# Optimization experiments

Hardware: AMD Instinct MI355X
Metric: run time of the kernel (lower is better)

The kernel has to match this reference:

```python
import jax, jax.numpy as jnp
import numpy as np

B, DIN, DOUT, DC, K, DB = 4096, 512, 512, 64, 16, 256
NEG = 0.01
LN_EPS = 1e-5

def _lrelu(v):
    return jnp.where(v >= 0, v, NEG * v)

def setup_inputs() -> dict:
    key = jax.random.key(0)
    ks = jax.random.split(key, 12)
    bound = 1.0 / np.sqrt(DIN)
    def u(k, shape, b):
        return jax.random.uniform(k, shape, jnp.float32, -b, b)
    return {
        "x": jax.random.normal(ks[0], (B, DIN), jnp.float32),
        "c": jax.random.normal(ks[1], (B, DC), jnp.float32),
        "ln_gamma": jnp.ones((DIN,), jnp.float32),
        "ln_beta": jnp.zeros((DIN,), jnp.float32),
        "w1": u(ks[2], (DC, DB), 1.0 / np.sqrt(DC)),
        "b1": u(ks[3], (DB,), 1.0 / np.sqrt(DC)),
        "wr": u(ks[4], (DB, DB), 1.0 / np.sqrt(DB)),
        "br": u(ks[5], (DB,), 1.0 / np.sqrt(DB)),
        "w2": u(ks[6], (DB, K), 1.0 / np.sqrt(DB)),
        "b2": u(ks[7], (K,), 1.0 / np.sqrt(DB)),
        "W": u(ks[8], (K, DIN, DOUT), bound),
        "bvec": u(ks[9], (K, DOUT), bound),
    }

def reference(x, c, ln_gamma, ln_beta, w1, b1, wr, br, w2, b2, W, bvec):
    # DenseActivation: LayerNorm + LeakyReLU (dropout_rate=0)
    mu = jnp.mean(x, axis=-1, keepdims=True)
    var = jnp.mean(jnp.square(x - mu), axis=-1, keepdims=True)
    xn = (x - mu) * jax.lax.rsqrt(var + LN_EPS) * ln_gamma + ln_beta
    a = _lrelu(xn)  # [B, DIN]
    # basis_functions(c): Linear -> 1 preactivation resnet block -> LeakyReLU -> Linear
    h = c @ w1 + b1                      # [B, DB]
    h = h + (_lrelu(h) @ wr + br)        # residual block (preactivation)
    h = _lrelu(h)                        # activate_output
    bf = h @ w2 + b2                     # [B, K]
    # out_b = x_b^T (sum_k bf_bk W_k) + bf_b @ bias ; reordered contraction
    xw = jnp.einsum("bi,kio->bko", a, W)       # [B, K, DOUT]
    out = jnp.einsum("bk,bko->bo", bf, xw)     # [B, DOUT]
    out = out + bf @ bvec
    return out
```

## Files before the change

### kernel.cpp

```cpp
#include <hip/hip_runtime.h>


#define LRELU(v) ((v) >= 0.f ? (v) : 0.01f * (v))

typedef _Float16 f16x8 __attribute__((ext_vector_type(8)));
typedef float f32x4 __attribute__((ext_vector_type(4)));

#define GL16(gp, lp) __builtin_amdgcn_global_load_lds(                      \
    (const __attribute__((address_space(1))) void*)(gp),                    \
    (__attribute__((address_space(3))) void*)(lp), 16, 0, 0)

#define MFMA16(a, b, c) __builtin_amdgcn_mfma_f32_16x16x32_f16((a), (b), (c), 0, 0, 0)

__global__ __launch_bounds__(256) void prep_kernel(
    const float* __restrict__ x, const float* __restrict__ gam,
    const float* __restrict__ bet, _Float16* __restrict__ a,
    const float* __restrict__ c, const float* __restrict__ w1,
    const float* __restrict__ b1, const float* __restrict__ wr,
    const float* __restrict__ br, const float* __restrict__ w2,
    const float* __restrict__ b2, float* __restrict__ bfo,
    const float* __restrict__ W, _Float16* __restrict__ Wt)
{
    __shared__ __align__(16) char smem[18432];
    int tid = threadIdx.x;
    int blk = blockIdx.x;

    if (blk < 512) {
        float* c_l  = (float*)smem;
        float* lr_l = (float*)(smem + 2048);
        float* h_l  = (float*)(smem + 10240);
        int b0 = blk * 8;

        for (int i = tid; i < 8 * 64; i += 256) c_l[i] = c[(size_t)b0 * 64 + i];

        float w1c[64];
#pragma unroll
        for (int u = 0; u < 64; ++u) w1c[u] = w1[u * 256 + tid];
        float b1s = b1[tid];
        __syncthreads();

        float h1[8];
#pragma unroll
        for (int r = 0; r < 8; ++r) h1[r] = b1s;
#pragma unroll
        for (int j4 = 0; j4 < 16; ++j4) {
#pragma unroll
            for (int r = 0; r < 8; ++r) {
                float4 cv = *(const float4*)&c_l[r * 64 + j4 * 4];
                h1[r] += cv.x * w1c[j4 * 4 + 0] + cv.y * w1c[j4 * 4 + 1] +
                         cv.z * w1c[j4 * 4 + 2] + cv.w * w1c[j4 * 4 + 3];
            }
        }
#pragma unroll
        for (int r = 0; r < 8; ++r) lr_l[r * 256 + tid] = LRELU(h1[r]);
        __syncthreads();

        float brv = br[tid];
        float h2[8];
#pragma unroll
        for (int r = 0; r < 8; ++r) h2[r] = h1[r] + brv;

#pragma unroll 1
        for (int jc = 0; jc < 8; ++jc) {
            float w8[32];
#pragma unroll
            for (int u = 0; u < 32; ++u) w8[u] = wr[(jc * 32 + u) * 256 + tid];
#pragma unroll
            for (int j4 = 0; j4 < 8; ++j4) {
#pragma unroll
                for (int r = 0; r < 8; ++r) {
                    float4 lv = *(const float4*)&lr_l[r * 256 + jc * 32 + j4 * 4];
                    h2[r] += lv.x * w8[j4 * 4 + 0] + lv.y * w8[j4 * 4 + 1] +
                             lv.z * w8[j4 * 4 + 2] + lv.w * w8[j4 * 4 + 3];
                }
            }
        }
#pragma unroll
        for (int r = 0; r < 8; ++r) h_l[r * 256 + tid] = LRELU(h2[r]);
        __syncthreads();

        if (tid < 128) {
            int r = tid >> 4, k = tid & 15;
            float s = b2[k];
#pragma unroll 1
            for (int qc = 0; qc < 8; ++qc) {
                float wv[32];
#pragma unroll
                for (int u = 0; u < 32; ++u) wv[u] = w2[(qc * 32 + u) * 16 + k];
#pragma unroll
                for (int q4 = 0; q4 < 8; ++q4) {
                    float4 hv = *(const float4*)&h_l[r * 256 + qc * 32 + q4 * 4];
                    s += hv.x * wv[q4 * 4 + 0] + hv.y * wv[q4 * 4 + 1] +
                         hv.z * wv[q4 * 4 + 2] + hv.w * wv[q4 * 4 + 3];
                }
            }
            bfo[(size_t)(b0 + r) * 16 + k] = s;
        }

    } else if (blk < 1536) {
        float* t = (float*)smem;
        int bid = blk - 512;
        int k  = bid >> 6;
        int it = (bid >> 3) & 7;
        int ot = bid & 7;
        int i0 = it * 64, o0 = ot * 64;

        int rr = tid >> 4, c4 = (tid & 15) * 4;
#pragma unroll
        for (int p = 0; p < 4; ++p) {
            int r = p * 16 + rr;
            float4 v = *(const float4*)&W[((size_t)(k * 512 + i0 + r)) * 512 + o0 + c4];
            t[r * 65 + c4 + 0] = v.x;
            t[r * 65 + c4 + 1] = v.y;
            t[r * 65 + c4 + 2] = v.z;
            t[r * 65 + c4 + 3] = v.w;
        }
        __syncthreads();

        int ol = tid >> 2, c0 = (tid & 3) * 16;
        _Float16 hb[16] __attribute__((aligned(16)));
#pragma unroll
        for (int u = 0; u < 16; ++u) hb[u] = (_Float16)t[(c0 + u) * 65 + ol];
        _Float16* dst = &Wt[(size_t)(o0 + ol) * 8192 + k * 512 + i0 + c0];
        *(float4*)dst       = *(const float4*)&hb[0];
        *(float4*)(dst + 8) = *(const float4*)&hb[8];

    } else {
        int lane = tid & 63;
        int row  = (blk - 1536) * 4 + (tid >> 6);
        const float* xr = x + (size_t)row * 512 + lane * 8;
        float4 v0 = *(const float4*)xr;
        float4 v1 = *(const float4*)(xr + 4);

        float s = v0.x + v0.y + v0.z + v0.w + v1.x + v1.y + v1.z + v1.w;
#pragma unroll
        for (int m = 1; m < 64; m <<= 1) s += __shfl_xor(s, m);
        float mean = s * (1.f / 512.f);

        float d, s2 = 0.f;
        d = v0.x - mean; s2 += d * d;
        d = v0.y - mean; s2 += d * d;
        d = v0.z - mean; s2 += d * d;
        d = v0.w - mean; s2 += d * d;
        d = v1.x - mean; s2 += d * d;
        d = v1.y - mean; s2 += d * d;
        d = v1.z - mean; s2 += d * d;
        d = v1.w - mean; s2 += d * d;
#pragma unroll
        for (int m = 1; m < 64; m <<= 1) s2 += __shfl_xor(s2, m);
        float rstd = rsqrtf(s2 * (1.f / 512.f) + 1e-5f);

        float4 g0 = *(const float4*)&gam[lane * 8];
        float4 g1 = *(const float4*)&gam[lane * 8 + 4];
        float4 b0 = *(const float4*)&bet[lane * 8];
        float4 b1v = *(const float4*)&bet[lane * 8 + 4];

        _Float16 o8[8] __attribute__((aligned(16)));
        float y;
        y = (v0.x - mean) * rstd * g0.x + b0.x;  y = LRELU(y); o8[0] = (_Float16)y;
        y = (v0.y - mean) * rstd * g0.y + b0.y;  y = LRELU(y); o8[1] = (_Float16)y;
        y = (v0.z - mean) * rstd * g0.z + b0.z;  y = LRELU(y); o8[2] = (_Float16)y;
        y = (v0.w - mean) * rstd * g0.w + b0.w;  y = LRELU(y); o8[3] = (_Float16)y;
        y = (v1.x - mean) * rstd * g1.x + b1v.x; y = LRELU(y); o8[4] = (_Float16)y;
        y = (v1.y - mean) * rstd * g1.y + b1v.y; y = LRELU(y); o8[5] = (_Float16)y;
        y = (v1.z - mean) * rstd * g1.z + b1v.z; y = LRELU(y); o8[6] = (_Float16)y;
        y = (v1.w - mean) * rstd * g1.w + b1v.w; y = LRELU(y); o8[7] = (_Float16)y;

        *(float4*)&a[(size_t)row * 512 + lane * 8] = *(const float4*)o8;
    }
}

template <int NSPLIT>
__global__ __launch_bounds__(512, 2) void gemm_kernel(
    const _Float16* __restrict__ A,
    const _Float16* __restrict__ Wt,
    const float* __restrict__ bfg,
    float* __restrict__ pout)
{
    constexpr int KTN = 16 / NSPLIT;
    constexpr int NT  = KTN * 8;

    __shared__ _Float16 As[2][256 * 64];
    __shared__ _Float16 Bs[2][256 * 64];

    const int tid = threadIdx.x;
    const int bid = blockIdx.x;
    const int split = bid % NSPLIT;
    const int mn  = bid / NSPLIT;
    const int n0  = (mn & 1) * 256;
    const int bm0 = (mn >> 1) * 256;
    const int kt0 = split * KTN;

    const int lane = tid & 63, wid = tid >> 6;
    const int wm = wid >> 2, wn = wid & 3;
    const int l16 = lane & 15, lg = lane >> 4;

    _Float16 s16[KTN][8];
#pragma unroll
    for (int kt = 0; kt < KTN; ++kt)
#pragma unroll
        for (int f = 0; f < 8; ++f)
            s16[kt][f] = (_Float16)
                bfg[(size_t)(bm0 + wm * 128 + f * 16 + l16) * 16 + kt0 + kt];

    const int brow = tid >> 3;
    const int bc   = tid & 7;
    const int swc  = bc ^ (brow & 7);
    const _Float16* aAs = A  + (size_t)(bm0 + brow) * 512  + swc * 8;
    const _Float16* aBs = Wt + (size_t)(n0  + brow) * 8192 + swc * 8;

    auto STAGE = [&](int t, int buf) {
        const int ka = (t & 7) * 64;
        const size_t kb = (size_t)(kt0 + (t >> 3)) * 512 + ka;
        char* la = (char*)&As[buf][0] + tid * 16;
        char* lb = (char*)&Bs[buf][0] + tid * 16;
#pragma unroll
        for (int p = 0; p < 4; ++p) {
            GL16(aAs + (size_t)(p * 64) * 512 + ka, la + p * 8192);
            GL16(aBs + (size_t)(p * 64) * 8192 + kb, lb + p * 8192);
        }
    };

    const int swr = l16 & 7;
    const int aRowByte = (wm * 128 + l16) * 128;
    const int bRowByte = (wn * 64 + l16) * 128;
    const int sw0 = ((0 + lg) ^ swr) << 4;
    const int sw1 = ((4 + lg) ^ swr) << 4;

    const f32x4 z4 = {0.f, 0.f, 0.f, 0.f};
    f32x4 acc[8][4];
#pragma unroll
    for (int f = 0; f < 8; ++f)
#pragma unroll
        for (int nf = 0; nf < 4; ++nf) acc[f][nf] = z4;

    STAGE(0, 0);
    STAGE(1, 1);
    asm volatile("s_waitcnt vmcnt(8)" ::: "memory");
    __builtin_amdgcn_s_barrier();
    __builtin_amdgcn_sched_barrier(0);

#pragma unroll
    for (int kt = 0; kt < KTN; ++kt) {
#pragma unroll 1
        for (int t2 = 0; t2 < 8; ++t2) {
            const int t = kt * 8 + t2;
            const int cur = t & 1;
            const char* Ab = (const char*)&As[cur][0];
            const char* Bb = (const char*)&Bs[cur][0];

            f16x8 b8[4][2];
#pragma unroll
            for (int nf = 0; nf < 4; ++nf) {
                b8[nf][0] = *(const f16x8*)(Bb + bRowByte + nf * 2048 + sw0);
                b8[nf][1] = *(const f16x8*)(Bb + bRowByte + nf * 2048 + sw1);
            }

#pragma unroll
            for (int q = 0; q < 4; ++q) {
                f16x8 a0k0 = *(const f16x8*)(Ab + aRowByte + (2 * q + 0) * 2048 + sw0);
                f16x8 a0k1 = *(const f16x8*)(Ab + aRowByte + (2 * q + 0) * 2048 + sw1);
                f16x8 a1k0 = *(const f16x8*)(Ab + aRowByte + (2 * q + 1) * 2048 + sw0);
                f16x8 a1k1 = *(const f16x8*)(Ab + aRowByte + (2 * q + 1) * 2048 + sw1);
                const _Float16 sc0 = s16[kt][2 * q + 0];
                const _Float16 sc1 = s16[kt][2 * q + 1];
                a0k0 *= sc0; a0k1 *= sc0;
                a1k0 *= sc1; a1k1 *= sc1;
                __builtin_amdgcn_s_setprio(1);
#pragma unroll
                for (int nf = 0; nf < 4; ++nf) {
                    acc[2 * q + 0][nf] = MFMA16(a0k0, b8[nf][0], acc[2 * q + 0][nf]);
                    acc[2 * q + 0][nf] = MFMA16(a0k1, b8[nf][1], acc[2 * q + 0][nf]);
                    acc[2 * q + 1][nf] = MFMA16(a1k0, b8[nf][0], acc[2 * q + 1][nf]);
                    acc[2 * q + 1][nf] = MFMA16(a1k1, b8[nf][1], acc[2 * q + 1][nf]);
                }
                __builtin_amdgcn_s_setprio(0);
            }

            __builtin_amdgcn_sched_barrier(0);
            __builtin_amdgcn_s_barrier();
            __builtin_amdgcn_sched_barrier(0);

            if (t + 2 < NT) {
                STAGE(t + 2, cur);
                asm volatile("s_waitcnt vmcnt(8)" ::: "memory");
            } else {
                asm volatile("s_waitcnt vmcnt(0)" ::: "memory");
            }
            __builtin_amdgcn_s_barrier();
            __builtin_amdgcn_sched_barrier(0);
        }
    }

    float* op = pout + (size_t)split * (4096 * 512);
#pragma unroll
    for (int f = 0; f < 8; ++f)
#pragma unroll
        for (int j = 0; j < 4; ++j) {
            const int grow = bm0 + wm * 128 + f * 16 + lg * 4 + j;
            float* orow = op + (size_t)grow * 512 + n0 + wn * 64 + l16;
#pragma unroll
            for (int nf = 0; nf < 4; ++nf)
                orow[nf * 16] = acc[f][nf][j];
        }
}

__global__ __launch_bounds__(256) void reduce_kernel(const float* __restrict__ p,
                                                     const float* __restrict__ bfg,
                                                     const float* __restrict__ bvec,
                                                     float* __restrict__ out,
                                                     int nsplit)
{
    size_t i = (size_t)blockIdx.x * 256 + threadIdx.x;
    const float4* p4 = (const float4*)p;
    float4 s = p4[i];
    for (int sp = 1; sp < nsplit; ++sp) {
        float4 v = p4[i + (size_t)sp * 524288];
        s.x += v.x; s.y += v.y; s.z += v.z; s.w += v.w;
    }
    int b = (int)(i >> 7);
    int c = (int)(i & 127);
    const float* bfr = bfg + (size_t)b * 16;
    const float4* bv4 = (const float4*)bvec;
#pragma unroll
    for (int k = 0; k < 16; ++k) {
        float bk = bfr[k];
        float4 v = bv4[k * 128 + c];
        s.x += bk * v.x; s.y += bk * v.y; s.z += bk * v.z; s.w += bk * v.w;
    }
    ((float4*)out)[i] = s;
}

extern "C" void kernel_launch(void* const* d_in, const int* in_sizes, int n_in,
                              void* d_out, int out_size, void* d_ws, size_t ws_size,
                              hipStream_t stream)
{
    const float* x    = (const float*)d_in[0];
    const float* c    = (const float*)d_in[1];
    const float* gam  = (const float*)d_in[2];
    const float* bet  = (const float*)d_in[3];
    const float* w1   = (const float*)d_in[4];
    const float* b1   = (const float*)d_in[5];
    const float* wr   = (const float*)d_in[6];
    const float* br   = (const float*)d_in[7];
    const float* w2   = (const float*)d_in[8];
    const float* b2   = (const float*)d_in[9];
    const float* W    = (const float*)d_in[10];
    const float* bvec = (const float*)d_in[11];
    float* out = (float*)d_out;

    const size_t outBytes  = (size_t)4096 * 512 * 4;
    const size_t miscBytes = (8u << 20) + (4u << 20) + (256u << 10);

    int nsplit = (ws_size >= 8 * outBytes + miscBytes) ? 8 : 4;

    char* ws = (char*)d_ws;
    size_t pbytes = (size_t)nsplit * outBytes;
    float*    part = (float*)ws;
    _Float16* Wt   = (_Float16*)(ws + pbytes);
    _Float16* af   = (_Float16*)(ws + pbytes + (8u << 20));
    float*    bf   = (float*)(ws + pbytes + (12u << 20));

    prep_kernel<<<dim3(2560), dim3(256), 0, stream>>>(
        x, gam, bet, af, c, w1, b1, wr, br, w2, b2, bf, W, Wt);

    if (nsplit == 8) {
        gemm_kernel<8><<<dim3(256), dim3(512), 0, stream>>>(af, Wt, bf, part);
    } else {
        gemm_kernel<4><<<dim3(128), dim3(512), 0, stream>>>(af, Wt, bf, part);
    }
    reduce_kernel<<<dim3(2048), dim3(256), 0, stream>>>(part, bf, bvec, out, nsplit);
}
```

Measured before the change: 92.08 us.

## Interleave next-tile global-to-LDS loads with MFMA phases inside the k-step

The inner k-step is split into four phases, one per pair of A fragments. Each phase has its own barriers, and the prefetch of tile t+2 into the current buffer is spread across them. B-tile loads start once every wave has finished reading B. A-tile row groups are overwritten only after the matching A fragments have been read. This aims to overlap global_load_lds traffic with MFMA work instead of issuing all loads in one burst after compute. The cost is several extra workgroup barriers per k-step and a tighter reliance on phase ordering being correct.

Result: slower. 94.07 us (+2.2%).

```diff
diff --git a/kernel.cpp b/kernel.cpp
--- a/kernel.cpp
+++ b/kernel.cpp
@@ -11,6 +11,10 @@
     (__attribute__((address_space(3))) void*)(lp), 16, 0, 0)
 
 #define MFMA16(a, b, c) __builtin_amdgcn_mfma_f32_16x16x32_f16((a), (b), (c), 0, 0, 0)
+
+#define BAR() do { __builtin_amdgcn_sched_barrier(0);                       \
+                   __builtin_amdgcn_s_barrier();                            \
+                   __builtin_amdgcn_sched_barrier(0); } while (0)
 
 __global__ __launch_bounds__(256) void prep_kernel(
     const float* __restrict__ x, const float* __restrict__ gam,
@@ -204,8 +208,7 @@
                 bfg[(size_t)(bm0 + wm * 128 + f * 16 + l16) * 16 + kt0 + kt];
 
     const int brow = tid >> 3;
-    const int bc   = tid & 7;
-    const int swc  = bc ^ (brow & 7);
+    const int swc  = (tid & 7) ^ (brow & 7);
     const _Float16* aAs = A  + (size_t)(bm0 + brow) * 512  + swc * 8;
     const _Float16* aBs = Wt + (size_t)(n0  + brow) * 8192 + swc * 8;
 
@@ -237,8 +240,38 @@
     STAGE(0, 0);
     STAGE(1, 1);
     asm volatile("s_waitcnt vmcnt(8)" ::: "memory");
-    __builtin_amdgcn_s_barrier();
-    __builtin_amdgcn_sched_barrier(0);
+    BAR();
+
+#define AREAD(q)                                                            \
+    xa = *(const f16x8*)(Ab + aRowByte + (2 * (q) + 0) * 2048 + sw0);       \
+    xb = *(const f16x8*)(Ab + aRowByte + (2 * (q) + 0) * 2048 + sw1);       \
+    xc = *(const f16x8*)(Ab + aRowByte + (2 * (q) + 1) * 2048 + sw0);       \
+    xd = *(const f16x8*)(Ab + aRowByte + (2 * (q) + 1) * 2048 + sw1);
+
+#define MFMAQ(q)                                                            \
+    {                                                                       \
+        const _Float16 sA = s16[kt][2 * (q) + 0];                           \
+        const _Float16 sB = s16[kt][2 * (q) + 1];                           \
+        xa *= sA; xb *= sA; xc *= sB; xd *= sB;                             \
+        __builtin_amdgcn_s_setprio(1);                                      \
+        acc[2*(q)+0][0] = MFMA16(xa, bA0, acc[2*(q)+0][0]);                 \
+        acc[2*(q)+0][0] = MFMA16(xb, bA1, acc[2*(q)+0][0]);                 \
+        acc[2*(q)+0][1] = MFMA16(xa, bB0, acc[2*(q)+0][1]);                 \
+        acc[2*(q)+0][1] = MFMA16(xb, bB1, acc[2*(q)+0][1]);                 \
+        acc[2*(q)+0][2] = MFMA16(xa, bC0, acc[2*(q)+0][2]);                 \
+        acc[2*(q)+0][2] = MFMA16(xb, bC1, acc[2*(q)+0][2]);                 \
+        acc[2*(q)+0][3] = MFMA16(xa, bD0, acc[2*(q)+0][3]);                 \
+        acc[2*(q)+0][3] = MFMA16(xb, bD1, acc[2*(q)+0][3]);                 \
+        acc[2*(q)+1][0] = MFMA16(xc, bA0, acc[2*(q)+1][0]);                 \
+        acc[2*(q)+1][0] = MFMA16(xd, bA1, acc[2*(q)+1][0]);                 \
+        acc[2*(q)+1][1] = MFMA16(xc, bB0, acc[2*(q)+1][1]);                 \
+        acc[2*(q)+1][1] = MFMA16(xd, bB1, acc[2*(q)+1][1]);                 \
+        acc[2*(q)+1][2] = MFMA16(xc, bC0, acc[2*(q)+1][2]);                 \
+        acc[2*(q)+1][2] = MFMA16(xd, bC1, acc[2*(q)+1][2]);                 \
+        acc[2*(q)+1][3] = MFMA16(xc, bD0, acc[2*(q)+1][3]);                 \
+        acc[2*(q)+1][3] = MFMA16(xd, bD1, acc[2*(q)+1][3]);                 \
+        __builtin_amdgcn_s_setprio(0);                                      \
+    }
 
 #pragma unroll
     for (int kt = 0; kt < KTN; ++kt) {
@@ -248,49 +281,65 @@
             const int cur = t & 1;
             const char* Ab = (const char*)&As[cur][0];
             const char* Bb = (const char*)&Bs[cur][0];
-
-            f16x8 b8[4][2];
-#pragma unroll
-            for (int nf = 0; nf < 4; ++nf) {
-                b8[nf][0] = *(const f16x8*)(Bb + bRowByte + nf * 2048 + sw0);
-                b8[nf][1] = *(const f16x8*)(Bb + bRowByte + nf * 2048 + sw1);
-            }
-
-#pragma unroll
-            for (int q = 0; q < 4; ++q) {
-                f16x8 a0k0 = *(const f16x8*)(Ab + aRowByte + (2 * q + 0) * 2048 + sw0);
-                f16x8 a0k1 = *(const f16x8*)(Ab + aRowByte + (2 * q + 0) * 2048 + sw1);
-                f16x8 a1k0 = *(const f16x8*)(Ab + aRowByte + (2 * q + 1) * 2048 + sw0);
-                f16x8 a1k1 = *(const f16x8*)(Ab + aRowByte + (2 * q + 1) * 2048 + sw1);
-                const _Float16 sc0 = s16[kt][2 * q + 0];
-                const _Float16 sc1 = s16[kt][2 * q + 1];
-                a0k0 *= sc0; a0k1 *= sc0;
-                a1k0 *= sc1; a1k1 *= sc1;
-                __builtin_amdgcn_s_setprio(1);
-#pragma unroll
-                for (int nf = 0; nf < 4; ++nf) {
-                    acc[2 * q + 0][nf] = MFMA16(a0k0, b8[nf][0], acc[2 * q + 0][nf]);
-                    acc[2 * q + 0][nf] = MFMA16(a0k1, b8[nf][1], acc[2 * q + 0][nf]);
-                    acc[2 * q + 1][nf] = MFMA16(a1k0, b8[nf][0], acc[2 * q + 1][nf]);
-                    acc[2 * q + 1][nf] = MFMA16(a1k1, b8[nf][1], acc[2 * q + 1][nf]);
-                }
-                __builtin_amdgcn_s_setprio(0);
-            }
-
-            __builtin_amdgcn_sched_barrier(0);
-            __builtin_amdgcn_s_barrier();
-            __builtin_amdgcn_sched_barrier(0);
-
-            if (t + 2 < NT) {
-                STAGE(t + 2, cur);
+            const int tt = t + 2;
+            const bool st = (tt < NT);
+            char* sAd = (char*)&As[cur][0] + tid * 16;
+            char* sBd = (char*)&Bs[cur][0] + tid * 16;
+            const int ka = (tt & 7) * 64;
+            const size_t kb = (size_t)(kt0 + (tt >> 3)) * 512 + ka;
+
+            f16x8 xa, xb, xc, xd;
+
+            f16x8 bA0 = *(const f16x8*)(Bb + bRowByte + 0 * 2048 + sw0);
+            f16x8 bA1 = *(const f16x8*)(Bb + bRowByte + 0 * 2048 + sw1);
+            f16x8 bB0 = *(const f16x8*)(Bb + bRowByte + 1 * 2048 + sw0);
+            f16x8 bB1 = *(const f16x8*)(Bb + bRowByte + 1 * 2048 + sw1);
+            f16x8 bC0 = *(const f16x8*)(Bb + bRowByte + 2 * 2048 + sw0);
+            f16x8 bC1 = *(const f16x8*)(Bb + bRowByte + 2 * 2048 + sw1);
+            f16x8 bD0 = *(const f16x8*)(Bb + bRowByte + 3 * 2048 + sw0);
+            f16x8 bD1 = *(const f16x8*)(Bb + bRowByte + 3 * 2048 + sw1);
+            AREAD(0);
+            BAR();
+            MFMAQ(0);
+            BAR();
+
+            AREAD(1);
+            if (st) {
+                GL16(aBs + (size_t)(0 * 64) * 8192 + kb, sBd + 0 * 8192);
+                GL16(aBs + (size_t)(1 * 64) * 8192 + kb, sBd + 1 * 8192);
+            }
+            BAR();
+            MFMAQ(1);
+            BAR();
+
+            AREAD(2);
+            if (st) {
+                GL16(aBs + (size_t)(2 * 64) * 8192 + kb, sBd + 2 * 8192);
+                GL16(aBs + (size_t)(3 * 64) * 8192 + kb, sBd + 3 * 8192);
+                GL16(aAs + (size_t)(0 * 64) * 512 + ka, sAd + 0 * 8192);
+                GL16(aAs + (size_t)(2 * 64) * 512 + ka, sAd + 2 * 8192);
+            }
+            BAR();
+            MFMAQ(2);
+            BAR();
+
+            AREAD(3);
+            BAR();
+            MFMAQ(3);
+            BAR();
+
+            if (st) {
+                GL16(aAs + (size_t)(1 * 64) * 512 + ka, sAd + 1 * 8192);
+                GL16(aAs + (size_t)(3 * 64) * 512 + ka, sAd + 3 * 8192);
                 asm volatile("s_waitcnt vmcnt(8)" ::: "memory");
             } else {
                 asm volatile("s_waitcnt vmcnt(0)" ::: "memory");
             }
-            __builtin_amdgcn_s_barrier();
-            __builtin_amdgcn_sched_barrier(0);
-        }
-    }
+            BAR();
+        }
+    }
+#undef AREAD
+#undef MFMAQ
 
     float* op = pout + (size_t)split * (4096 * 512);
 #pragma unroll
```

## Shrink GEMM tiles to 128x128 and reuse A tile across basis functions

Applied to the files above, without the earlier changes.

The GEMM kernel moves from 256x256 tiles with 512 threads and a double-buffered global_load_lds pipeline to 128x128 tiles with 256 threads, four blocks per CU, and four times as many blocks. The K loop is reordered so each 64-wide slice of the activation tile is loaded once and reused across all basis functions in the split. The explicit prefetch and vmcnt pipelining is replaced by single-buffered loads bracketed by __syncthreads. The intent is higher occupancy and fewer redundant A loads. In exchange it loses load/compute overlap within a block and raises B-tile traffic per output, since smaller tiles mean less reuse.

Result: slower. 239.8 us (+160.4%).

```diff
diff --git a/kernel.cpp b/kernel.cpp
--- a/kernel.cpp
+++ b/kernel.cpp
@@ -171,133 +171,105 @@
 }
 
 template <int NSPLIT>
-__global__ __launch_bounds__(512, 2) void gemm_kernel(
+__global__ __launch_bounds__(256, 4) void gemm_kernel(
     const _Float16* __restrict__ A,
     const _Float16* __restrict__ Wt,
     const float* __restrict__ bfg,
     float* __restrict__ pout)
 {
     constexpr int KTN = 16 / NSPLIT;
-    constexpr int NT  = KTN * 8;
-
-    __shared__ _Float16 As[2][256 * 64];
-    __shared__ _Float16 Bs[2][256 * 64];
+
+    __shared__ _Float16 As[128 * 64];
+    __shared__ _Float16 Bs[128 * 64];
 
     const int tid = threadIdx.x;
     const int bid = blockIdx.x;
     const int split = bid % NSPLIT;
     const int mn  = bid / NSPLIT;
-    const int n0  = (mn & 1) * 256;
-    const int bm0 = (mn >> 1) * 256;
+    const int n0  = (mn & 3) * 128;
+    const int bm0 = (mn >> 2) * 128;
     const int kt0 = split * KTN;
 
     const int lane = tid & 63, wid = tid >> 6;
-    const int wm = wid >> 2, wn = wid & 3;
+    const int wm = wid >> 1, wn = wid & 1;
     const int l16 = lane & 15, lg = lane >> 4;
 
-    _Float16 s16[KTN][8];
+    _Float16 s16[KTN][4];
 #pragma unroll
     for (int kt = 0; kt < KTN; ++kt)
 #pragma unroll
-        for (int f = 0; f < 8; ++f)
+        for (int f = 0; f < 4; ++f)
             s16[kt][f] = (_Float16)
-                bfg[(size_t)(bm0 + wm * 128 + f * 16 + l16) * 16 + kt0 + kt];
-
-    const int brow = tid >> 3;
-    const int bc   = tid & 7;
-    const int swc  = bc ^ (brow & 7);
-    const _Float16* aAs = A  + (size_t)(bm0 + brow) * 512  + swc * 8;
-    const _Float16* aBs = Wt + (size_t)(n0  + brow) * 8192 + swc * 8;
-
-    auto STAGE = [&](int t, int buf) {
-        const int ka = (t & 7) * 64;
-        const size_t kb = (size_t)(kt0 + (t >> 3)) * 512 + ka;
-        char* la = (char*)&As[buf][0] + tid * 16;
-        char* lb = (char*)&Bs[buf][0] + tid * 16;
-#pragma unroll
-        for (int p = 0; p < 4; ++p) {
-            GL16(aAs + (size_t)(p * 64) * 512 + ka, la + p * 8192);
-            GL16(aBs + (size_t)(p * 64) * 8192 + kb, lb + p * 8192);
-        }
-    };
+                bfg[(size_t)(bm0 + wm * 64 + f * 16 + l16) * 16 + kt0 + kt];
+
+    const int srow = tid >> 3;
+    const int swc  = (tid & 7) ^ (srow & 7);
+    const _Float16* aAs = A  + (size_t)(bm0 + srow) * 512  + swc * 8;
+    const _Float16* aBs = Wt + (size_t)(n0  + srow) * 8192 + swc * 8;
+    char* lA = (char*)As + tid * 16;
+    char* lB = (char*)Bs + tid * 16;
 
     const int swr = l16 & 7;
-    const int aRowByte = (wm * 128 + l16) * 128;
-    const int bRowByte = (wn * 64 + l16) * 128;
+    const int aRow = (wm * 64 + l16) * 128;
+    const int bRow = (wn * 64 + l16) * 128;
     const int sw0 = ((0 + lg) ^ swr) << 4;
     const int sw1 = ((4 + lg) ^ swr) << 4;
 
     const f32x4 z4 = {0.f, 0.f, 0.f, 0.f};
-    f32x4 acc[8][4];
-#pragma unroll
-    for (int f = 0; f < 8; ++f)
+    f32x4 acc[4][4];
+#pragma unroll
+    for (int f = 0; f < 4; ++f)
 #pragma unroll
         for (int nf = 0; nf < 4; ++nf) acc[f][nf] = z4;
 
-    STAGE(0, 0);
-    STAGE(1, 1);
-    asm volatile("s_waitcnt vmcnt(8)" ::: "memory");
-    __builtin_amdgcn_s_barrier();
-    __builtin_amdgcn_sched_barrier(0);
-
-#pragma unroll
-    for (int kt = 0; kt < KTN; ++kt) {
 #pragma unroll 1
-        for (int t2 = 0; t2 < 8; ++t2) {
-            const int t = kt * 8 + t2;
-            const int cur = t & 1;
-            const char* Ab = (const char*)&As[cur][0];
-            const char* Bb = (const char*)&Bs[cur][0];
-
-            f16x8 b8[4][2];
+    for (int ks = 0; ks < 8; ++ks) {
+        const int ig = ks * 64;
+#pragma unroll
+        for (int kt = 0; kt < KTN; ++kt) {
+            if (kt == 0) {
+#pragma unroll
+                for (int p = 0; p < 4; ++p)
+                    GL16(aAs + (size_t)(p * 32) * 512 + ig, lA + p * 4096);
+            }
+            const size_t kb = (size_t)(kt0 + kt) * 512 + ig;
+#pragma unroll
+            for (int p = 0; p < 4; ++p)
+                GL16(aBs + (size_t)(p * 32) * 8192 + kb, lB + p * 4096);
+            __syncthreads();
+
+            const char* Ab = (const char*)As;
+            const char* Bb = (const char*)Bs;
+            f16x8 bb[4][2];
 #pragma unroll
             for (int nf = 0; nf < 4; ++nf) {
-                b8[nf][0] = *(const f16x8*)(Bb + bRowByte + nf * 2048 + sw0);
-                b8[nf][1] = *(const f16x8*)(Bb + bRowByte + nf * 2048 + sw1);
-            }
-
-#pragma unroll
-            for (int q = 0; q < 4; ++q) {
-                f16x8 a0k0 = *(const f16x8*)(Ab + aRowByte + (2 * q + 0) * 2048 + sw0);
-                f16x8 a0k1 = *(const f16x8*)(Ab + aRowByte + (2 * q + 0) * 2048 + sw1);
-                f16x8 a1k0 = *(const f16x8*)(Ab + aRowByte + (2 * q + 1) * 2048 + sw0);
-                f16x8 a1k1 = *(const f16x8*)(Ab + aRowByte + (2 * q + 1) * 2048 + sw1);
-                const _Float16 sc0 = s16[kt][2 * q + 0];
-                const _Float16 sc1 = s16[kt][2 * q + 1];
-                a0k0 *= sc0; a0k1 *= sc0;
-                a1k0 *= sc1; a1k1 *= sc1;
+                bb[nf][0] = *(const f16x8*)(Bb + bRow + nf * 2048 + sw0);
+                bb[nf][1] = *(const f16x8*)(Bb + bRow + nf * 2048 + sw1);
+            }
+#pragma unroll
+            for (int f = 0; f < 4; ++f) {
+                f16x8 a0 = *(const f16x8*)(Ab + aRow + f * 2048 + sw0);
+                f16x8 a1 = *(const f16x8*)(Ab + aRow + f * 2048 + sw1);
+                const _Float16 s = s16[kt][f];
+                a0 *= s; a1 *= s;
                 __builtin_amdgcn_s_setprio(1);
 #pragma unroll
                 for (int nf = 0; nf < 4; ++nf) {
-                    acc[2 * q + 0][nf] = MFMA16(a0k0, b8[nf][0], acc[2 * q + 0][nf]);
-                    acc[2 * q + 0][nf] = MFMA16(a0k1, b8[nf][1], acc[2 * q + 0][nf]);
-                    acc[2 * q + 1][nf] = MFMA16(a1k0, b8[nf][0], acc[2 * q + 1][nf]);
-                    acc[2 * q + 1][nf] = MFMA16(a1k1, b8[nf][1], acc[2 * q + 1][nf]);
+                    acc[f][nf] = MFMA16(a0, bb[nf][0], acc[f][nf]);
+                    acc[f][nf] = MFMA16(a1, bb[nf][1], acc[f][nf]);
                 }
                 __builtin_amdgcn_s_setprio(0);
             }
-
-            __builtin_amdgcn_sched_barrier(0);
-            __builtin_amdgcn_s_barrier();
-            __builtin_amdgcn_sched_barrier(0);
-
-            if (t + 2 < NT) {
-                STAGE(t + 2, cur);
-                asm volatile("s_waitcnt vmcnt(8)" ::: "memory");
-            } else {
-                asm volatile("s_waitcnt vmcnt(0)" ::: "memory");
-            }
-            __builtin_amdgcn_s_barrier();
-            __builtin_amdgcn_sched_barrier(0);
+            __syncthreads();
         }
     }
 
     float* op = pout + (size_t)split * (4096 * 512);
 #pragma unroll
-    for (int f = 0; f < 8; ++f)
+    for (int f = 0; f < 4; ++f)
 #pragma unroll
         for (int j = 0; j < 4; ++j) {
-            const int grow = bm0 + wm * 128 + f * 16 + lg * 4 + j;
+            const int grow = bm0 + wm * 64 + f * 16 + lg * 4 + j;
             float* orow = op + (size_t)grow * 512 + n0 + wn * 64 + l16;
 #pragma unroll
             for (int nf = 0; nf < 4; ++nf)
@@ -365,9 +337,9 @@
         x, gam, bet, af, c, w1, b1, wr, br, w2, b2, bf, W, Wt);
 
     if (nsplit == 8) {
-        gemm_kernel<8><<<dim3(256), dim3(512), 0, stream>>>(af, Wt, bf, part);
+        gemm_kernel<8><<<dim3(1024), dim3(256), 0, stream>>>(af, Wt, bf, part);
     } else {
-        gemm_kernel<4><<<dim3(128), dim3(512), 0, stream>>>(af, Wt, bf, part);
+        gemm_kernel<4><<<dim3(512), dim3(256), 0, stream>>>(af, Wt, bf, part);
     }
     reduce_kernel<<<dim3(2048), dim3(256), 0, stream>>>(part, bf, bvec, out, nsplit);
 }
```
